# Performance work log

Measured on AMD Instinct MI355X. Metric: run time of the kernel, lower is better.

## Reference

```python
import jax, jax.numpy as jnp
import numpy as np

N_NODES = 100000
N_EDGES = 1600000
DIM = 128
N_SEEDS = 15000


def _gcn_stack(edges, x, Ws):
    """Multi-layer GCN with sym-normalized edge-list aggregation, residual, ReLU.
    edges: [2, E] int; x: [N, d] float; Ws: list of [d, d] weights."""
    n = x.shape[0]
    loop = jnp.arange(n, dtype=edges.dtype)
    src = jnp.concatenate([edges[0], loop])  # add self-loops
    dst = jnp.concatenate([edges[1], loop])
    deg = jax.ops.segment_sum(jnp.ones(src.shape, x.dtype), dst, num_segments=n)
    dinv = jax.lax.rsqrt(deg)  # deg >= 1 thanks to self-loops
    norm = dinv[src] * dinv[dst]  # [E+N]
    for W in Ws:
        h = x @ W                                   # [N, d] dense transform
        msg = norm[:, None] * h[src]                # gather + scale, [E+N, d]
        agg = jax.ops.segment_sum(msg, dst, num_segments=n)  # scatter-add
        x = jax.nn.relu(agg + h)                    # residual + activation
    return x


def setup_inputs() -> dict:
    key = jax.random.key(0)
    ks = jax.random.split(key, 8)
    scale = 1.0 / np.sqrt(DIM)
    return {
        "sr_ent_seeds": jax.random.randint(ks[0], (N_SEEDS,), 0, N_NODES),
        "tg_ent_seeds": jax.random.randint(ks[1], (N_SEEDS,), 0, N_NODES),
        "edges_sr": jax.random.randint(ks[2], (2, N_EDGES), 0, N_NODES),
        "edges_tg": jax.random.randint(ks[3], (2, N_EDGES), 0, N_NODES),
        "embedding_sr": jax.random.normal(ks[4], (N_NODES, DIM), jnp.float32),
        "embedding_tg": jax.random.normal(ks[5], (N_NODES, DIM), jnp.float32),
        "W0": jax.random.normal(ks[6], (DIM, DIM), jnp.float32) * scale,
        "W1": jax.random.normal(ks[7], (DIM, DIM), jnp.float32) * scale,
    }


def reference(sr_ent_seeds, tg_ent_seeds, edges_sr, edges_tg,
              embedding_sr, embedding_tg, W0, W1):
    Ws = [W0, W1]
    sr_ent_hid = _gcn_stack(edges_sr, embedding_sr, Ws)
    tg_ent_hid = _gcn_stack(edges_tg, embedding_tg, Ws)
    sr_seed_hid = sr_ent_hid[sr_ent_seeds]
    tg_seed_hid = tg_ent_hid[tg_ent_seeds]
    return (sr_seed_hid, tg_seed_hid, sr_ent_hid, tg_ent_hid)
```

## Files before the change

kernel.cpp:

```cpp
#include <hip/hip_runtime.h>

#define NN 100000
#define NE 1600000
#define NT (2 * NN)
#define ET (2 * NE)
#define DIM 128
#define NS 15000
#define SB2 ((NT + 255) / 256)
#define PAD 136
#define NRANGE 8
#define RSZ (NT / NRANGE)
#define CH 32
#define CI4 (ET / 4 / CH)
#define NE4 (NE / 4)

typedef __attribute__((ext_vector_type(8))) short frag_ab;
typedef __attribute__((ext_vector_type(4))) float frag_cd;
typedef __attribute__((ext_vector_type(4))) int i4;

__device__ __forceinline__ unsigned short f2bf(float f) {
    unsigned int u = __float_as_uint(f);
    u += 0x7fff + ((u >> 16) & 1);
    return (unsigned short)(u >> 16);
}
__device__ __forceinline__ float bflo(unsigned int u) { return __uint_as_float(u << 16); }
__device__ __forceinline__ float bfhi(unsigned int u) { return __uint_as_float(u & 0xffff0000u); }

__global__ __launch_bounds__(1024) void hist_k(const int* __restrict__ e_sr,
                                               const int* __restrict__ e_tg,
                                               int* __restrict__ P) {
    __shared__ int lc[RSZ];
    const int r = blockIdx.x & (NRANGE - 1);
    const int c = blockIdx.x >> 3;
    const int lo = r * RSZ;
    for (int i = threadIdx.x; i < RSZ; i += 1024) lc[i] = 0;
    __syncthreads();
    const int base = c * CI4;
    for (int v = threadIdx.x; v < CI4; v += 1024) {
        i4 d4;
        if (c < 16) {
            d4 = __builtin_nontemporal_load((const i4*)e_sr + NE4 + base + v);
        } else {
            d4 = __builtin_nontemporal_load((const i4*)e_tg + base + v);
            d4 += NN;
        }
#pragma unroll
        for (int j = 0; j < 4; ++j) {
            const int t = d4[j] - lo;
            if ((unsigned)t < RSZ) atomicAdd(&lc[t], 1);
        }
    }
    __syncthreads();
    for (int i = threadIdx.x; i < RSZ; i += 1024) P[c * NT + lo + i] = lc[i];
}

__global__ __launch_bounds__(256) void reduce_k(const int* __restrict__ P,
                                                int* __restrict__ cnt,
                                                float* __restrict__ dinv) {
    const int i = blockIdx.x * 256 + threadIdx.x;
    if (i >= NT) return;
    int s = 0;
#pragma unroll
    for (int c = 0; c < CH; ++c) s += P[c * NT + i];
    cnt[i] = s;
    dinv[i] = rsqrtf((float)(s + 1));
}

__global__ __launch_bounds__(256) void scanA_k(const int* __restrict__ cnt, int* bsum) {
    __shared__ int s[256];
    const int t = threadIdx.x;
    const int i = blockIdx.x * 256 + t;
    s[t] = (i < NT) ? cnt[i] : 0;
    __syncthreads();
    for (int off = 128; off > 0; off >>= 1) {
        if (t < off) s[t] += s[t + off];
        __syncthreads();
    }
    if (t == 0) bsum[blockIdx.x] = s[0];
}

__global__ __launch_bounds__(1024) void scanB_k(int* bsum, int* row_ptr) {
    __shared__ int s[1024];
    const int t = threadIdx.x;
    const int v = (t < SB2) ? bsum[t] : 0;
    s[t] = v;
    __syncthreads();
    for (int off = 1; off < 1024; off <<= 1) {
        int add = (t >= off) ? s[t - off] : 0;
        __syncthreads();
        s[t] += add;
        __syncthreads();
    }
    if (t < SB2) bsum[t] = s[t] - v;
    if (t == SB2 - 1) row_ptr[NT] = s[t];
}

__global__ __launch_bounds__(256) void scanC_k(const int* __restrict__ cnt,
                                               const int* __restrict__ bsum,
                                               int* row_ptr) {
    __shared__ int s[256];
    const int t = threadIdx.x;
    const int i = blockIdx.x * 256 + t;
    const int v = (i < NT) ? cnt[i] : 0;
    s[t] = v;
    __syncthreads();
    for (int off = 1; off < 256; off <<= 1) {
        int add = (t >= off) ? s[t - off] : 0;
        __syncthreads();
        s[t] += add;
        __syncthreads();
    }
    if (i < NT) row_ptr[i] = bsum[blockIdx.x] + s[t] - v;
}

__global__ __launch_bounds__(256) void base_k(int* __restrict__ P,
                                              const int* __restrict__ row_ptr) {
    const int i = blockIdx.x * 256 + threadIdx.x;
    if (i >= NT) return;
    int run = row_ptr[i];
#pragma unroll
    for (int c = 0; c < CH; ++c) {
        const int v = P[c * NT + i];
        P[c * NT + i] = run;
        run += v;
    }
}

__global__ __launch_bounds__(1024) void fillp_k(const int* __restrict__ e_sr,
                                                const int* __restrict__ e_tg,
                                                const int* __restrict__ P,
                                                int* __restrict__ csr_src) {
    __shared__ int cur[RSZ];
    const int r = blockIdx.x & (NRANGE - 1);
    const int c = blockIdx.x >> 3;
    const int lo = r * RSZ;
    for (int i = threadIdx.x; i < RSZ; i += 1024) cur[i] = P[c * NT + lo + i];
    __syncthreads();
    const int base = c * CI4;
    for (int v = threadIdx.x; v < CI4; v += 1024) {
        i4 s4, d4;
        if (c < 16) {
            s4 = __builtin_nontemporal_load((const i4*)e_sr + base + v);
            d4 = __builtin_nontemporal_load((const i4*)e_sr + NE4 + base + v);
        } else {
            s4 = __builtin_nontemporal_load((const i4*)e_tg + base + v - NE4);
            d4 = __builtin_nontemporal_load((const i4*)e_tg + base + v);
            s4 += NN;
            d4 += NN;
        }
#pragma unroll
        for (int j = 0; j < 4; ++j) {
            const int t = d4[j] - lo;
            if ((unsigned)t < RSZ) {
                const int pos = atomicAdd(&cur[t], 1);
                csr_src[pos] = s4[j];
            }
        }
    }
}

__global__ __launch_bounds__(256) void convX_k(const float* __restrict__ emb_sr,
                                               const float* __restrict__ emb_tg,
                                               unsigned short* __restrict__ xb) {
    const int i = blockIdx.x * 256 + threadIdx.x;
    if (i >= NT * 32) return;
    const int node = i >> 5;
    float4 v = (node < NN) ? ((const float4*)emb_sr)[i]
                           : ((const float4*)emb_tg)[i - NN * 32];
    ushort4 o;
    o.x = f2bf(v.x); o.y = f2bf(v.y); o.z = f2bf(v.z); o.w = f2bf(v.w);
    ((ushort4*)xb)[i] = o;
}

__global__ __launch_bounds__(256) void convW_k(const float* __restrict__ W,
                                               unsigned short* __restrict__ wt) {
    int i = blockIdx.x * 256 + threadIdx.x;
    if (i >= DIM * DIM) return;
    const int n = i & 127, k = i >> 7;
    wt[n * DIM + k] = f2bf(W[k * DIM + n]);
}

__global__ __launch_bounds__(256) void gemm_mfma_k(const unsigned short* __restrict__ Xb,
                                                   const unsigned short* __restrict__ Wt,
                                                   const float* __restrict__ dinv,
                                                   unsigned short* __restrict__ Gb) {
    __shared__ unsigned short xs[64 * PAD];
    __shared__ unsigned short ws[128 * PAD];
    const int tid = threadIdx.x;
    const int row0 = blockIdx.x * 64;

    for (int i = tid; i < 128 * 16; i += 256) {
        const int r = i >> 4, o = i & 15;
        *(uint4*)&ws[r * PAD + o * 8] = *(const uint4*)&Wt[r * DIM + o * 8];
    }
    for (int i = tid; i < 64 * 16; i += 256) {
        const int r = i >> 4, o = i & 15;
        int gr = row0 + r; if (gr >= NT) gr = NT - 1;
        *(uint4*)&xs[r * PAD + o * 8] = *(const uint4*)&Xb[gr * DIM + o * 8];
    }
    __syncthreads();

    const int wave = tid >> 6;
    const int lane = tid & 63;
    const int m = lane & 15;
    const int quad = lane >> 4;
    const int rbase = wave * 16;

    frag_cd acc[8];
#pragma unroll
    for (int ct = 0; ct < 8; ct++) acc[ct] = (frag_cd){0.f, 0.f, 0.f, 0.f};

#pragma unroll
    for (int ks = 0; ks < 4; ks++) {
        const frag_ab a = *(const frag_ab*)&xs[(rbase + m) * PAD + ks * 32 + quad * 8];
#pragma unroll
        for (int ct = 0; ct < 8; ct++) {
            const frag_ab b = *(const frag_ab*)&ws[(ct * 16 + m) * PAD + ks * 32 + quad * 8];
            acc[ct] = __builtin_amdgcn_mfma_f32_16x16x32_bf16(a, b, acc[ct], 0, 0, 0);
        }
    }

#pragma unroll
    for (int r = 0; r < 4; r++) {
        const int grow = row0 + rbase + quad * 4 + r;
        if (grow < NT) {
            const float dv = dinv[grow];
#pragma unroll
            for (int ct = 0; ct < 8; ct++)
                Gb[grow * DIM + ct * 16 + m] = f2bf(dv * acc[ct][r]);
        }
    }
}

template <bool OUT_BF16>
__global__ __launch_bounds__(256) void pull_k(const int* __restrict__ row_ptr,
                                              const int* __restrict__ csr_src,
                                              const float* __restrict__ dinv,
                                              const unsigned short* __restrict__ Gb,
                                              float* __restrict__ outf,
                                              unsigned short* __restrict__ outb) {
    const int node = (blockIdx.x * 256 + threadIdx.x) >> 6;
    if (node >= NT) return;
    const int lane = threadIdx.x & 63;
    const unsigned int* __restrict__ G2 = (const unsigned int*)Gb;

    const int beg = row_ptr[node];
    const int end = row_ptr[node + 1];
    const float d = dinv[node];
    const float sq = 1.0f / d;

    const unsigned int gu = G2[node * 64 + lane];
    float sx = bflo(gu);
    float sy = bfhi(gu);
    const float hx = sx * sq;
    const float hy = sy * sq;

    for (int base = beg; base < end; base += 64) {
        int rem = end - base; if (rem > 64) rem = 64;
        const int sl = (lane < rem) ? csr_src[base + lane] : 0;
        int j = 0;
        for (; j + 4 <= rem; j += 4) {
            const int s0 = __shfl(sl, j + 0);
            const int s1 = __shfl(sl, j + 1);
            const int s2 = __shfl(sl, j + 2);
            const int s3 = __shfl(sl, j + 3);
            const unsigned int m0 = G2[s0 * 64 + lane];
            const unsigned int m1 = G2[s1 * 64 + lane];
            const unsigned int m2 = G2[s2 * 64 + lane];
            const unsigned int m3 = G2[s3 * 64 + lane];
            sx += bflo(m0) + bflo(m1) + bflo(m2) + bflo(m3);
            sy += bfhi(m0) + bfhi(m1) + bfhi(m2) + bfhi(m3);
        }
        for (; j < rem; ++j) {
            const int s = __shfl(sl, j);
            const unsigned int mu = G2[s * 64 + lane];
            sx += bflo(mu);
            sy += bfhi(mu);
        }
    }
    const float ax = fmaxf(d * sx + hx, 0.f);
    const float ay = fmaxf(d * sy + hy, 0.f);
    if (OUT_BF16) {
        ((unsigned int*)outb)[node * 64 + lane] =
            (unsigned int)f2bf(ax) | ((unsigned int)f2bf(ay) << 16);
    } else {
        float2 o; o.x = ax; o.y = ay;
        ((float2*)outf)[node * 64 + lane] = o;
    }
}

__global__ __launch_bounds__(256) void gather_k(const int* __restrict__ seeds,
                                                const float* __restrict__ ent,
                                                float* __restrict__ out, int node_off) {
    const int gid = blockIdx.x * 256 + threadIdx.x;
    const int s = gid >> 5;
    if (s >= NS) return;
    const int q = gid & 31;
    ((float4*)out)[s * 32 + q] =
        ((const float4*)ent)[(seeds[s] + node_off) * 32 + q];
}

extern "C" void kernel_launch(void* const* d_in, const int* in_sizes, int n_in,
                              void* d_out, int out_size, void* d_ws, size_t ws_size,
                              hipStream_t stream) {
    const int* sr_seeds = (const int*)d_in[0];
    const int* tg_seeds = (const int*)d_in[1];
    const int* edges_sr = (const int*)d_in[2];
    const int* edges_tg = (const int*)d_in[3];
    const float* emb_sr = (const float*)d_in[4];
    const float* emb_tg = (const float*)d_in[5];
    const float* W0 = (const float*)d_in[6];
    const float* W1 = (const float*)d_in[7];
    float* out = (float*)d_out;

    int* cnt = (int*)d_ws;
    float* dinv = (float*)(cnt + 200704);
    int* row_ptr = (int*)(dinv + 200704);
    int* bsum = row_ptr + 200704;
    int* csr_src = bsum + 1024;
    unsigned short* wt0 = (unsigned short*)(csr_src + ET);
    unsigned short* wt1 = wt0 + DIM * DIM;
    unsigned short* hb = wt1 + DIM * DIM;
    int* P = (int*)hb;

    float* sr_seed_out = out;
    float* tg_seed_out = out + (long long)NS * DIM;
    float* ent = out + (long long)2 * NS * DIM;
    unsigned short* xb = (unsigned short*)ent;

    const int gGemm = (NT + 63) / 64;
    const int gPull = NT / 4;
    const int gElem = (NT * 32 + 255) / 256;

    convW_k<<<(DIM * DIM + 255) / 256, 256, 0, stream>>>(W0, wt0);
    convW_k<<<(DIM * DIM + 255) / 256, 256, 0, stream>>>(W1, wt1);

    hist_k<<<NRANGE * CH, 1024, 0, stream>>>(edges_sr, edges_tg, P);
    reduce_k<<<SB2, 256, 0, stream>>>(P, cnt, dinv);
    scanA_k<<<SB2, 256, 0, stream>>>(cnt, bsum);
    scanB_k<<<1, 1024, 0, stream>>>(bsum, row_ptr);
    scanC_k<<<SB2, 256, 0, stream>>>(cnt, bsum, row_ptr);
    base_k<<<SB2, 256, 0, stream>>>(P, row_ptr);
    fillp_k<<<NRANGE * CH, 1024, 0, stream>>>(edges_sr, edges_tg, P, csr_src);

    convX_k<<<gElem, 256, 0, stream>>>(emb_sr, emb_tg, xb);

    gemm_mfma_k<<<gGemm, 256, 0, stream>>>(xb, wt0, dinv, hb);
    pull_k<true><<<gPull, 256, 0, stream>>>(row_ptr, csr_src, dinv, hb, nullptr, xb);
    gemm_mfma_k<<<gGemm, 256, 0, stream>>>(xb, wt1, dinv, hb);
    pull_k<false><<<gPull, 256, 0, stream>>>(row_ptr, csr_src, dinv, hb, ent, nullptr);

    const int gSeed = (NS * 32 + 255) / 256;
    gather_k<<<gSeed, 256, 0, stream>>>(sr_seeds, ent, sr_seed_out, 0);
    gather_k<<<gSeed, 256, 0, stream>>>(tg_seeds, ent, tg_seed_out, NN);
}
```

Measured before the change: 642.3 us.

## Fuse aggregation and GEMM per layer by reordering to aggregate-then-transform

```diff
diff --git a/kernel.cpp b/kernel.cpp
--- a/kernel.cpp
+++ b/kernel.cpp
@@ -39,9 +39,9 @@
     for (int v = threadIdx.x; v < CI4; v += 1024) {
         i4 d4;
         if (c < 16) {
-            d4 = __builtin_nontemporal_load((const i4*)e_sr + NE4 + base + v);
+            d4 = *((const i4*)e_sr + NE4 + base + v);
         } else {
-            d4 = __builtin_nontemporal_load((const i4*)e_tg + base + v);
+            d4 = *((const i4*)e_tg + base + v);
             d4 += NN;
         }
 #pragma unroll
@@ -54,29 +54,27 @@
     for (int i = threadIdx.x; i < RSZ; i += 1024) P[c * NT + lo + i] = lc[i];
 }
 
-__global__ __launch_bounds__(256) void reduce_k(const int* __restrict__ P,
-                                                int* __restrict__ cnt,
-                                                float* __restrict__ dinv) {
-    const int i = blockIdx.x * 256 + threadIdx.x;
-    if (i >= NT) return;
-    int s = 0;
-#pragma unroll
-    for (int c = 0; c < CH; ++c) s += P[c * NT + i];
-    cnt[i] = s;
-    dinv[i] = rsqrtf((float)(s + 1));
-}
-
-__global__ __launch_bounds__(256) void scanA_k(const int* __restrict__ cnt, int* bsum) {
-    __shared__ int s[256];
+__global__ __launch_bounds__(256) void reduceA_k(const int* __restrict__ P,
+                                                 int* __restrict__ cnt,
+                                                 float* __restrict__ dinv,
+                                                 int* __restrict__ bsum) {
+    __shared__ int sh[256];
     const int t = threadIdx.x;
     const int i = blockIdx.x * 256 + t;
-    s[t] = (i < NT) ? cnt[i] : 0;
+    int s = 0;
+    if (i < NT) {
+#pragma unroll
+        for (int c = 0; c < CH; ++c) s += P[c * NT + i];
+        cnt[i] = s;
+        dinv[i] = rsqrtf((float)(s + 1));
+    }
+    sh[t] = s;
     __syncthreads();
     for (int off = 128; off > 0; off >>= 1) {
-        if (t < off) s[t] += s[t + off];
-        __syncthreads();
-    }
-    if (t == 0) bsum[blockIdx.x] = s[0];
+        if (t < off) sh[t] += sh[t + off];
+        __syncthreads();
+    }
+    if (t == 0) bsum[blockIdx.x] = sh[0];
 }
 
 __global__ __launch_bounds__(1024) void scanB_k(int* bsum, int* row_ptr) {
@@ -95,9 +93,10 @@
     if (t == SB2 - 1) row_ptr[NT] = s[t];
 }
 
-__global__ __launch_bounds__(256) void scanC_k(const int* __restrict__ cnt,
-                                               const int* __restrict__ bsum,
-                                               int* row_ptr) {
+__global__ __launch_bounds__(256) void scanCbase_k(const int* __restrict__ cnt,
+                                                   const int* __restrict__ bsum,
+                                                   int* __restrict__ row_ptr,
+                                                   int* __restrict__ P) {
     __shared__ int s[256];
     const int t = threadIdx.x;
     const int i = blockIdx.x * 256 + t;
@@ -110,19 +109,16 @@
         s[t] += add;
         __syncthreads();
     }
-    if (i < NT) row_ptr[i] = bsum[blockIdx.x] + s[t] - v;
-}
-
-__global__ __launch_bounds__(256) void base_k(int* __restrict__ P,
-                                              const int* __restrict__ row_ptr) {
-    const int i = blockIdx.x * 256 + threadIdx.x;
-    if (i >= NT) return;
-    int run = row_ptr[i];
-#pragma unroll
-    for (int c = 0; c < CH; ++c) {
-        const int v = P[c * NT + i];
-        P[c * NT + i] = run;
-        run += v;
+    if (i < NT) {
+        const int rp = bsum[blockIdx.x] + s[t] - v;
+        row_ptr[i] = rp;
+        int run = rp;
+#pragma unroll
+        for (int c = 0; c < CH; ++c) {
+            const int pv = P[c * NT + i];
+            P[c * NT + i] = run;
+            run += pv;
+        }
     }
 }
 
@@ -140,11 +136,11 @@
     for (int v = threadIdx.x; v < CI4; v += 1024) {
         i4 s4, d4;
         if (c < 16) {
-            s4 = __builtin_nontemporal_load((const i4*)e_sr + base + v);
-            d4 = __builtin_nontemporal_load((const i4*)e_sr + NE4 + base + v);
+            s4 = *((const i4*)e_sr + base + v);
+            d4 = *((const i4*)e_sr + NE4 + base + v);
         } else {
-            s4 = __builtin_nontemporal_load((const i4*)e_tg + base + v - NE4);
-            d4 = __builtin_nontemporal_load((const i4*)e_tg + base + v);
+            s4 = *((const i4*)e_tg + base + v - NE4);
+            d4 = *((const i4*)e_tg + base + v);
             s4 += NN;
             d4 += NN;
         }
@@ -159,17 +155,18 @@
     }
 }
 
-__global__ __launch_bounds__(256) void convX_k(const float* __restrict__ emb_sr,
-                                               const float* __restrict__ emb_tg,
-                                               unsigned short* __restrict__ xb) {
+__global__ __launch_bounds__(256) void convX2_k(const float* __restrict__ emb_sr,
+                                                const float* __restrict__ emb_tg,
+                                                const float* __restrict__ dinv,
+                                                unsigned int* __restrict__ xq) {
     const int i = blockIdx.x * 256 + threadIdx.x;
-    if (i >= NT * 32) return;
-    const int node = i >> 5;
-    float4 v = (node < NN) ? ((const float4*)emb_sr)[i]
-                           : ((const float4*)emb_tg)[i - NN * 32];
-    ushort4 o;
-    o.x = f2bf(v.x); o.y = f2bf(v.y); o.z = f2bf(v.z); o.w = f2bf(v.w);
-    ((ushort4*)xb)[i] = o;
+    if (i >= NT * 64) return;
+    const int node = i >> 6;
+    const float d = dinv[node];
+    float2 v = (node < NN) ? ((const float2*)emb_sr)[i]
+                           : ((const float2*)emb_tg)[i - NN * 64];
+    const unsigned int p = (unsigned int)f2bf(d * v.x) | ((unsigned int)f2bf(d * v.y) << 16);
+    __builtin_nontemporal_store(p, &xq[i]);
 }
 
 __global__ __launch_bounds__(256) void convW_k(const float* __restrict__ W,
@@ -180,28 +177,72 @@
     wt[n * DIM + k] = f2bf(W[k * DIM + n]);
 }
 
-__global__ __launch_bounds__(256) void gemm_mfma_k(const unsigned short* __restrict__ Xb,
-                                                   const unsigned short* __restrict__ Wt,
-                                                   const float* __restrict__ dinv,
-                                                   unsigned short* __restrict__ Gb) {
-    __shared__ unsigned short xs[64 * PAD];
-    __shared__ unsigned short ws[128 * PAD];
+template <bool FINAL>
+__global__ __launch_bounds__(256, 4) void layer_k(const int* __restrict__ row_ptr,
+                                                  const int* __restrict__ csr_src,
+                                                  const float* __restrict__ dinv,
+                                                  const unsigned int* __restrict__ X2,
+                                                  const unsigned short* __restrict__ Wt,
+                                                  float* __restrict__ outf,
+                                                  unsigned short* __restrict__ outq) {
+    __shared__ unsigned short zs[64 * PAD];
     const int tid = threadIdx.x;
-    const int row0 = blockIdx.x * 64;
-
-    for (int i = tid; i < 128 * 16; i += 256) {
-        const int r = i >> 4, o = i & 15;
-        *(uint4*)&ws[r * PAD + o * 8] = *(const uint4*)&Wt[r * DIM + o * 8];
-    }
-    for (int i = tid; i < 64 * 16; i += 256) {
-        const int r = i >> 4, o = i & 15;
-        int gr = row0 + r; if (gr >= NT) gr = NT - 1;
-        *(uint4*)&xs[r * PAD + o * 8] = *(const uint4*)&Xb[gr * DIM + o * 8];
-    }
-    __syncthreads();
-
     const int wave = tid >> 6;
     const int lane = tid & 63;
+    const int node0 = blockIdx.x * 64;
+
+    for (int r = wave * 16; r < wave * 16 + 16; ++r) {
+        const int node = node0 + r;
+        unsigned int zpack = 0;
+        if (node < NT) {
+            const int beg = row_ptr[node];
+            const int end = row_ptr[node + 1];
+            float sx = 0.f, sy = 0.f;
+            for (int base = beg; base < end; base += 64) {
+                int rem = end - base; if (rem > 64) rem = 64;
+                const int sl = (lane < rem)
+                    ? __builtin_nontemporal_load(&csr_src[base + lane]) : 0;
+                int j = 0;
+                for (; j + 8 <= rem; j += 8) {
+                    const int s0 = __shfl(sl, j + 0);
+                    const int s1 = __shfl(sl, j + 1);
+                    const int s2 = __shfl(sl, j + 2);
+                    const int s3 = __shfl(sl, j + 3);
+                    const int s4 = __shfl(sl, j + 4);
+                    const int s5 = __shfl(sl, j + 5);
+                    const int s6 = __shfl(sl, j + 6);
+                    const int s7 = __shfl(sl, j + 7);
+                    const unsigned int m0 = X2[s0 * 64 + lane];
+                    const unsigned int m1 = X2[s1 * 64 + lane];
+                    const unsigned int m2 = X2[s2 * 64 + lane];
+                    const unsigned int m3 = X2[s3 * 64 + lane];
+                    const unsigned int m4 = X2[s4 * 64 + lane];
+                    const unsigned int m5 = X2[s5 * 64 + lane];
+                    const unsigned int m6 = X2[s6 * 64 + lane];
+                    const unsigned int m7 = X2[s7 * 64 + lane];
+                    sx += bflo(m0) + bflo(m1) + bflo(m2) + bflo(m3)
+                        + bflo(m4) + bflo(m5) + bflo(m6) + bflo(m7);
+                    sy += bfhi(m0) + bfhi(m1) + bfhi(m2) + bfhi(m3)
+                        + bfhi(m4) + bfhi(m5) + bfhi(m6) + bfhi(m7);
+                }
+                for (; j < rem; ++j) {
+                    const int s = __shfl(sl, j);
+                    const unsigned int mu = X2[s * 64 + lane];
+                    sx += bflo(mu);
+                    sy += bfhi(mu);
+                }
+            }
+            const float d = dinv[node];
+            const float cf = d + 1.0f / d;
+            const unsigned int xt = X2[node * 64 + lane];
+            const float zx = d * sx + cf * bflo(xt);
+            const float zy = d * sy + cf * bfhi(xt);
+            zpack = (unsigned int)f2bf(zx) | ((unsigned int)f2bf(zy) << 16);
+        }
+        *(unsigned int*)&zs[r * PAD + lane * 2] = zpack;
+    }
+    __syncthreads();
+
     const int m = lane & 15;
     const int quad = lane >> 4;
     const int rbase = wave * 16;
@@ -212,80 +253,31 @@
 
 #pragma unroll
     for (int ks = 0; ks < 4; ks++) {
-        const frag_ab a = *(const frag_ab*)&xs[(rbase + m) * PAD + ks * 32 + quad * 8];
+        const frag_ab a = *(const frag_ab*)&zs[(rbase + m) * PAD + ks * 32 + quad * 8];
 #pragma unroll
         for (int ct = 0; ct < 8; ct++) {
-            const frag_ab b = *(const frag_ab*)&ws[(ct * 16 + m) * PAD + ks * 32 + quad * 8];
+            const frag_ab b = *(const frag_ab*)&Wt[(ct * 16 + m) * DIM + ks * 32 + quad * 8];
             acc[ct] = __builtin_amdgcn_mfma_f32_16x16x32_bf16(a, b, acc[ct], 0, 0, 0);
         }
     }
 
 #pragma unroll
     for (int r = 0; r < 4; r++) {
-        const int grow = row0 + rbase + quad * 4 + r;
+        const int grow = node0 + rbase + quad * 4 + r;
         if (grow < NT) {
-            const float dv = dinv[grow];
-#pragma unroll
-            for (int ct = 0; ct < 8; ct++)
-                Gb[grow * DIM + ct * 16 + m] = f2bf(dv * acc[ct][r]);
-        }
-    }
-}
-
-template <bool OUT_BF16>
-__global__ __launch_bounds__(256) void pull_k(const int* __restrict__ row_ptr,
-                                              const int* __restrict__ csr_src,
-                                              const float* __restrict__ dinv,
-                                              const unsigned short* __restrict__ Gb,
-                                              float* __restrict__ outf,
-                                              unsigned short* __restrict__ outb) {
-    const int node = (blockIdx.x * 256 + threadIdx.x) >> 6;
-    if (node >= NT) return;
-    const int lane = threadIdx.x & 63;
-    const unsigned int* __restrict__ G2 = (const unsigned int*)Gb;
-
-    const int beg = row_ptr[node];
-    const int end = row_ptr[node + 1];
-    const float d = dinv[node];
-    const float sq = 1.0f / d;
-
-    const unsigned int gu = G2[node * 64 + lane];
-    float sx = bflo(gu);
-    float sy = bfhi(gu);
-    const float hx = sx * sq;
-    const float hy = sy * sq;
-
-    for (int base = beg; base < end; base += 64) {
-        int rem = end - base; if (rem > 64) rem = 64;
-        const int sl = (lane < rem) ? csr_src[base + lane] : 0;
-        int j = 0;
-        for (; j + 4 <= rem; j += 4) {
-            const int s0 = __shfl(sl, j + 0);
-            const int s1 = __shfl(sl, j + 1);
-            const int s2 = __shfl(sl, j + 2);
-            const int s3 = __shfl(sl, j + 3);
-            const unsigned int m0 = G2[s0 * 64 + lane];
-            const unsigned int m1 = G2[s1 * 64 + lane];
-            const unsigned int m2 = G2[s2 * 64 + lane];
-            const unsigned int m3 = G2[s3 * 64 + lane];
-            sx += bflo(m0) + bflo(m1) + bflo(m2) + bflo(m3);
-            sy += bfhi(m0) + bfhi(m1) + bfhi(m2) + bfhi(m3);
-        }
-        for (; j < rem; ++j) {
-            const int s = __shfl(sl, j);
-            const unsigned int mu = G2[s * 64 + lane];
-            sx += bflo(mu);
-            sy += bfhi(mu);
-        }
-    }
-    const float ax = fmaxf(d * sx + hx, 0.f);
-    const float ay = fmaxf(d * sy + hy, 0.f);
-    if (OUT_BF16) {
-        ((unsigned int*)outb)[node * 64 + lane] =
-            (unsigned int)f2bf(ax) | ((unsigned int)f2bf(ay) << 16);
-    } else {
-        float2 o; o.x = ax; o.y = ay;
-        ((float2*)outf)[node * 64 + lane] = o;
+            if (FINAL) {
+#pragma unroll
+                for (int ct = 0; ct < 8; ct++)
+                    __builtin_nontemporal_store(fmaxf(acc[ct][r], 0.f),
+                                                &outf[grow * DIM + ct * 16 + m]);
+            } else {
+                const float dv = dinv[grow];
+#pragma unroll
+                for (int ct = 0; ct < 8; ct++)
+                    __builtin_nontemporal_store(f2bf(dv * fmaxf(acc[ct][r], 0.f)),
+                                                &outq[grow * DIM + ct * 16 + m]);
+            }
+        }
     }
 }
 
@@ -322,33 +314,31 @@
     unsigned short* wt1 = wt0 + DIM * DIM;
     unsigned short* hb = wt1 + DIM * DIM;
     int* P = (int*)hb;
+    unsigned int* xq1 = (unsigned int*)hb;
 
     float* sr_seed_out = out;
     float* tg_seed_out = out + (long long)NS * DIM;
     float* ent = out + (long long)2 * NS * DIM;
-    unsigned short* xb = (unsigned short*)ent;
-
-    const int gGemm = (NT + 63) / 64;
-    const int gPull = NT / 4;
-    const int gElem = (NT * 32 + 255) / 256;
+    unsigned int* xq0 = (unsigned int*)ent;
+
+    const int gLayer = (NT + 63) / 64;
+    const int gConv = (NT * 64) / 256;
 
     convW_k<<<(DIM * DIM + 255) / 256, 256, 0, stream>>>(W0, wt0);
     convW_k<<<(DIM * DIM + 255) / 256, 256, 0, stream>>>(W1, wt1);
 
     hist_k<<<NRANGE * CH, 1024, 0, stream>>>(edges_sr, edges_tg, P);
-    reduce_k<<<SB2, 256, 0, stream>>>(P, cnt, dinv);
-    scanA_k<<<SB2, 256, 0, stream>>>(cnt, bsum);
+    reduceA_k<<<SB2, 256, 0, stream>>>(P, cnt, dinv, bsum);
     scanB_k<<<1, 1024, 0, stream>>>(bsum, row_ptr);
-    scanC_k<<<SB2, 256, 0, stream>>>(cnt, bsum, row_ptr);
-    base_k<<<SB2, 256, 0, stream>>>(P, row_ptr);
+    scanCbase_k<<<SB2, 256, 0, stream>>>(cnt, bsum, row_ptr, P);
     fillp_k<<<NRANGE * CH, 1024, 0, stream>>>(edges_sr, edges_tg, P, csr_src);
 
-    convX_k<<<gElem, 256, 0, stream>>>(emb_sr, emb_tg, xb);
-
-    gemm_mfma_k<<<gGemm, 256, 0, stream>>>(xb, wt0, dinv, hb);
-    pull_k<true><<<gPull, 256, 0, stream>>>(row_ptr, csr_src, dinv, hb, nullptr, xb);
-    gemm_mfma_k<<<gGemm, 256, 0, stream>>>(xb, wt1, dinv, hb);
-    pull_k<false><<<gPull, 256, 0, stream>>>(row_ptr, csr_src, dinv, hb, ent, nullptr);
+    convX2_k<<<gConv, 256, 0, stream>>>(emb_sr, emb_tg, dinv, xq0);
+
+    layer_k<false><<<gLayer, 256, 0, stream>>>(row_ptr, csr_src, dinv, xq0, wt0,
+                                               nullptr, (unsigned short*)xq1);
+    layer_k<true><<<gLayer, 256, 0, stream>>>(row_ptr, csr_src, dinv, xq1, wt1,
+                                              ent, nullptr);
 
     const int gSeed = (NS * 32 + 255) / 256;
     gather_k<<<gSeed, 256, 0, stream>>>(sr_seeds, ent, sr_seed_out, 0);
```

Result: slower. 860.3 us (+34.0%).
